# Kernel optimization log

Hardware: AMD Instinct MI355X
Metric: run time of the kernel (lower is better)

## Reference

```python
import jax, jax.numpy as jnp
import numpy as np
import math

B, L, D = 2, 2048, 512
H, HD = 8, 64                      # num_heads, head_dim = D // H
NG = D * (D - 1) // 2              # SO(D) generator count = 130816


def setup_inputs() -> dict:
    key = jax.random.key(0)
    ks = jax.random.split(key, 8)
    x = jax.random.normal(ks[0], (B, L, D), jnp.float32)
    # additive causal mask [L, L]
    mask = jnp.where(jnp.tril(jnp.ones((L, L), bool)), 0.0, -1e9).astype(jnp.float32)
    coef = lambda k: jax.random.normal(k, (NG,), jnp.float32) * 0.1
    basis = lambda k: jax.random.normal(k, (HD, HD), jnp.float32) * 0.1
    return {
        "x": x, "mask": mask,
        "coef_q": coef(ks[1]), "coef_k": coef(ks[2]),
        "coef_v": coef(ks[3]), "coef_o": coef(ks[4]),
        "bias_q": jnp.zeros((D,), jnp.float32), "bias_k": jnp.zeros((D,), jnp.float32),
        "bias_v": jnp.zeros((D,), jnp.float32), "bias_o": jnp.zeros((D,), jnp.float32),
        "basis_q": basis(ks[5]), "basis_k": basis(ks[6]),
    }


def _make_W(coefs):
    # W = I + sum_i coef_i * G_i, with G_i the antisymmetric basis (row-major i<j).
    iu = jnp.triu_indices(D, k=1)
    A = jnp.zeros((D, D), coefs.dtype).at[iu].set(coefs)
    return A - A.T + jnp.eye(D, dtype=coefs.dtype)


def _proj(x, coefs, bias):
    # F.linear(x, W, b) = x @ W.T + b
    return x @ _make_W(coefs).T + bias


def _invariants(t, basis):
    # t: [B, H, L, HD] -> concat(norm, t @ basis.T)[..., :HD]
    norm = jnp.linalg.norm(t, axis=-1, keepdims=True)
    ip = jnp.einsum('bhld,nd->bhln', t, basis)
    return jnp.concatenate([norm, ip], axis=-1)[..., :HD]


def reference(x, mask, coef_q, coef_k, coef_v, coef_o,
              bias_q, bias_k, bias_v, bias_o, basis_q, basis_k):
    split = lambda t: t.reshape(B, L, H, HD).transpose(0, 2, 1, 3)  # [B,H,L,HD]
    Q = split(_proj(x, coef_q, bias_q))
    K = split(_proj(x, coef_k, bias_k))
    V = split(_proj(x, coef_v, bias_v))
    Qi = _invariants(Q, basis_q)
    Ki = _invariants(K, basis_k)
    scores = jnp.einsum('bhld,bhmd->bhlm', Qi, Ki) / math.sqrt(HD) + mask
    attn = jax.nn.softmax(scores, axis=-1)
    out = jnp.einsum('bhlm,bhmd->bhld', attn, V)
    out = out.transpose(0, 2, 1, 3).reshape(B, L, D)
    return _proj(out, coef_o, bias_o)
```

## Files before the change

### kernel.cpp

```cpp
#include <hip/hip_runtime.h>
#include <hip/hip_bf16.h>
#include <math.h>

#define D_ 512
#define B_ 2
#define L_ 2048
#define H_ 8
#define HD_ 64

typedef __attribute__((ext_vector_type(8))) short short8;
typedef __attribute__((ext_vector_type(4))) float f32x4;

__device__ __forceinline__ ushort f2bf(float f) {
  __hip_bfloat16 h = __float2bfloat16(f);
  return *(ushort*)&h;
}
__device__ __forceinline__ float bf2f(ushort u) {
  unsigned int v = ((unsigned int)u) << 16;
  union { unsigned int u; float f; } c; c.u = v; return c.f;
}
__device__ __forceinline__ int swz(int row, int col) {
  return row*64 + (((col>>3) ^ (row&7))<<3) + (col&7);
}
__device__ __forceinline__ int tri_idx(int i, int j) {
  return i*(D_-1) - (i*(i-1))/2 + (j - i - 1);
}

#define GLL16(g, l) __builtin_amdgcn_global_load_lds( \
    (const __attribute__((address_space(1))) void*)(g), \
    (__attribute__((address_space(3))) void*)(l), 16, 0, 0)
#define GLL4(g, l) __builtin_amdgcn_global_load_lds( \
    (const __attribute__((address_space(1))) void*)(g), \
    (__attribute__((address_space(3))) void*)(l), 4, 0, 0)

__global__ void prep_kernel(const float* __restrict__ x,
                            const float* __restrict__ cq, const float* __restrict__ ck,
                            const float* __restrict__ cv, const float* __restrict__ co,
                            const float* __restrict__ basq, const float* __restrict__ bask,
                            ushort* __restrict__ xb, ushort* __restrict__ Wb,
                            ushort* __restrict__ Bq, ushort* __restrict__ Bk) {
  int blk = blockIdx.x, tid = threadIdx.x;
  if (blk < 2048) {
    int i = (blk*256 + tid)*4;
    float4 v = *(const float4*)(x + i);
    ushort4 o = make_ushort4(f2bf(v.x), f2bf(v.y), f2bf(v.z), f2bf(v.w));
    *(ushort4*)(xb + i) = o;
  } else if (blk < 6144) {
    int e = (blk-2048)*256 + tid;
    int m = e >> 18, n = (e>>9)&511, k = e&511;
    const float* cf = (m==0)?cq:(m==1)?ck:(m==2)?cv:co;
    float v = (k>n) ? cf[tri_idx(n,k)] : (k<n) ? -cf[tri_idx(k,n)] : 0.f;
    Wb[e] = f2bf(v);
  } else {
    int e = (blk-6144)*256 + tid;
    int which = e >> 12, ee = e & 4095;
    int n = ee >> 6, d = ee & 63;
    const float* bs = which ? bask : basq;
    float v = (n==0) ? 0.f : bs[(n-1)*64 + d];
    (which ? Bk : Bq)[ee] = f2bf(v);
  }
}

__global__ __launch_bounds__(256) void proj_kernel(
    const ushort* __restrict__ Xb, const float* __restrict__ Xf,
    const ushort* __restrict__ Wb,
    const float* __restrict__ bq, const float* __restrict__ bk,
    const float* __restrict__ bv, const float* __restrict__ bo,
    const ushort* __restrict__ Basq, const ushort* __restrict__ Bask,
    ushort* __restrict__ Qi_bf, float* __restrict__ Nq,
    ushort* __restrict__ Ki_bf, float* __restrict__ Nk,
    ushort* __restrict__ Vt_g, float* __restrict__ OutF,
    int mode_override)
{
  __shared__ ushort BufA[4096];
  __shared__ ushort BufB[4096];

  const int tid = threadIdx.x;
  const int lane = tid & 63, w = tid >> 6;
  const int lr = lane & 15, lg = lane >> 4;
  const int by = blockIdx.y;
  const int mode = (mode_override >= 0) ? mode_override : (by >> 6);
  const int mb   = (mode_override >= 0) ? by : (by & 63);
  const int h = blockIdx.x;
  const int n0 = h*64, m0 = mb*64;
  const ushort* Wm = Wb + (size_t)mode*262144;
  const float* bias = (mode==0)?bq:(mode==1)?bk:(mode==2)?bv:bo;

  f32x4 acc[4] = {};
  for (int k0 = 0; k0 < 512; k0 += 64) {
    __syncthreads();
    #pragma unroll
    for (int i = 0; i < 2; ++i) {
      int idx = tid + 256*i;
      int row = idx >> 3, c = idx & 7;
      *(short8*)&BufA[swz(row, c*8)] = *(const short8*)(Xb + (size_t)(m0+row)*512 + k0 + c*8);
      *(short8*)&BufB[swz(row, c*8)] = *(const short8*)(Wm + (size_t)(n0+row)*512 + k0 + c*8);
    }
    __syncthreads();
    short8 af[2];
    #pragma unroll
    for (int ks = 0; ks < 2; ++ks)
      af[ks] = *(const short8*)&BufA[swz(w*16+lr, (ks*4+lg)*8)];
    #pragma unroll
    for (int nb = 0; nb < 4; ++nb) {
      f32x4 a = acc[nb];
      #pragma unroll
      for (int ks = 0; ks < 2; ++ks) {
        short8 bfr = *(const short8*)&BufB[swz(nb*16+lr, (ks*4+lg)*8)];
        a = __builtin_amdgcn_mfma_f32_16x16x32_bf16(af[ks], bfr, a, 0,0,0);
      }
      acc[nb] = a;
    }
  }

  float bias4[4];
  #pragma unroll
  for (int nb = 0; nb < 4; ++nb) bias4[nb] = bias[n0 + nb*16 + lr];
  float q[4][4];
  #pragma unroll
  for (int nb = 0; nb < 4; ++nb)
    #pragma unroll
    for (int r = 0; r < 4; ++r) {
      size_t m = m0 + w*16 + lg*4 + r;
      size_t idx = m*512 + n0 + nb*16 + lr;
      float ex = Xf ? Xf[idx] : bf2f(Xb[idx]);
      q[nb][r] = ex + acc[nb][r] + bias4[nb];
    }

  if (mode == 2) {
    #pragma unroll
    for (int nb = 0; nb < 4; ++nb) {
      ushort4 o = make_ushort4(f2bf(q[nb][0]), f2bf(q[nb][1]), f2bf(q[nb][2]), f2bf(q[nb][3]));
      int b = m0 >> 11, l0 = (m0 & 2047) + w*16 + lg*4;
      size_t idx = (size_t)(b*8 + h)*131072 + (size_t)(nb*16 + lr)*2048 + l0;
      *(ushort4*)(Vt_g + idx) = o;
    }
    return;
  }
  if (mode == 3) {
    #pragma unroll
    for (int nb = 0; nb < 4; ++nb)
      #pragma unroll
      for (int r = 0; r < 4; ++r) {
        size_t m = m0 + w*16 + lg*4 + r;
        OutF[m*512 + n0 + nb*16 + lr] = q[nb][r];
      }
    return;
  }

  const float scale = (mode == 0) ? 0.125f : 1.0f;
  float norm[4];
  #pragma unroll
  for (int r = 0; r < 4; ++r) {
    float s = 0.f;
    #pragma unroll
    for (int nb = 0; nb < 4; ++nb) s = fmaf(q[nb][r], q[nb][r], s);
    s += __shfl_xor(s, 1, 16);
    s += __shfl_xor(s, 2, 16);
    s += __shfl_xor(s, 4, 16);
    s += __shfl_xor(s, 8, 16);
    norm[r] = sqrtf(s);
  }
  __syncthreads();
  {
    const ushort* Bsrc = (mode==0) ? Basq : Bask;
    #pragma unroll
    for (int i = 0; i < 2; ++i) {
      int idx = tid + 256*i;
      int row = idx >> 3, c = idx & 7;
      *(short8*)&BufB[swz(row, c*8)] = *(const short8*)(Bsrc + row*64 + c*8);
    }
  }
  #pragma unroll
  for (int nb = 0; nb < 4; ++nb)
    #pragma unroll
    for (int r = 0; r < 4; ++r)
      BufA[swz(w*16 + lg*4 + r, nb*16 + lr)] = f2bf(q[nb][r]);
  __syncthreads();

  f32x4 acc2[4] = {};
  short8 af2[2];
  #pragma unroll
  for (int ks = 0; ks < 2; ++ks)
    af2[ks] = *(const short8*)&BufA[swz(w*16+lr, (ks*4+lg)*8)];
  #pragma unroll
  for (int nb = 0; nb < 4; ++nb) {
    f32x4 a = acc2[nb];
    #pragma unroll
    for (int ks = 0; ks < 2; ++ks) {
      short8 bfr = *(const short8*)&BufB[swz(nb*16+lr, (ks*4+lg)*8)];
      a = __builtin_amdgcn_mfma_f32_16x16x32_bf16(af2[ks], bfr, a, 0,0,0);
    }
    acc2[nb] = a;
  }

  ushort* Qdst = (mode==0) ? Qi_bf : Ki_bf;
  float*  Ndst = (mode==0) ? Nq : Nk;
  int b = m0 >> 11;
  #pragma unroll
  for (int nb = 0; nb < 4; ++nb)
    #pragma unroll
    for (int r = 0; r < 4; ++r) {
      int ninv = nb*16 + lr;
      int l = (m0 & 2047) + w*16 + lg*4 + r;
      float v = acc2[nb][r] * scale;
      if (ninv == 0) v = 0.f;
      Qdst[((size_t)(b*8 + h)*2048 + l)*64 + ninv] = f2bf(v);
      if (lr == 0 && nb == 0) Ndst[(size_t)(b*8 + h)*2048 + l] = norm[r] * scale;
    }
}

__device__ __forceinline__ void stage_kv(const ushort* __restrict__ Kg,
                                         const ushort* __restrict__ Vg,
                                         const float* __restrict__ Nkg,
                                         ushort* Ksb, ushort* Vsb, float* Nkb,
                                         int w, int lane) {
  const int r8 = lane >> 3;
  const int cx = (lane & 7) ^ r8;
  #pragma unroll
  for (int s = 0; s < 2; ++s) {
    const int seg = w*2 + s;
    const int row = seg*8 + r8;
    GLL16(Kg + (size_t)row*64 + cx*8,   (char*)Ksb + seg*1024);
    GLL16(Vg + (size_t)row*2048 + cx*8, (char*)Vsb + seg*1024);
  }
  if (w == 0) GLL4(Nkg + lane, Nkb);
}

__global__ __launch_bounds__(256) void attn_kernel(
    const ushort* __restrict__ Qi_bf, const float* __restrict__ Nq,
    const ushort* __restrict__ Ki_bf, const float* __restrict__ Nk,
    const ushort* __restrict__ Vt_g, ushort* __restrict__ AO_bf)
{
  __shared__ ushort Ks[2][4096], Vt[2][4096], Pl[4096];
  __shared__ float NkS[2][64];

  const int tid = threadIdx.x;
  const int lane = tid & 63, w = tid >> 6;
  const int lr = lane & 15, lg = lane >> 4;
  const int blk = blockIdx.x;
  const int g  = blk >> 4;
  const int bh = blk & 15;
  const int qb = (g < 16) ? (31 - g) : (g - 16);
  const int b = bh >> 3, h = bh & 7;
  const ushort* Kg0 = Ki_bf + (size_t)bh*2048*64;
  const ushort* Vg0 = Vt_g + (size_t)bh*131072;
  const float*  Nkg = Nk + (size_t)bh*2048;
  const int prow = w*16 + lr;
  const int qg0 = qb*64;

  const ushort* qrow = Qi_bf + ((size_t)bh*2048 + qg0 + w*16 + lr)*64;
  short8 qf[2];
  qf[0] = *(const short8*)(qrow + lg*8);
  qf[1] = *(const short8*)(qrow + 32 + lg*8);
  const float nq = Nq[(size_t)bh*2048 + qg0 + w*16 + lr];

  float m_i = -1e30f, l_i = 0.f;
  f32x4 accO[4] = {};

  stage_kv(Kg0, Vg0, Nkg, Ks[0], Vt[0], NkS[0], w, lane);
  __syncthreads();

  for (int jb = 0; jb <= qb; ++jb) {
    const int cur = jb & 1;
    if (jb < qb)
      stage_kv(Kg0 + (size_t)(jb+1)*4096, Vg0 + (jb+1)*64, Nkg + (jb+1)*64,
               Ks[cur^1], Vt[cur^1], NkS[cur^1], w, lane);

    f32x4 sf[4];
    __builtin_amdgcn_s_setprio(1);
    #pragma unroll
    for (int cb = 0; cb < 4; ++cb) {
      f32x4 a = {0.f,0.f,0.f,0.f};
      #pragma unroll
      for (int ks = 0; ks < 2; ++ks) {
        short8 kfr = *(const short8*)&Ks[cur][swz(cb*16+lr, (ks*4+lg)*8)];
        a = __builtin_amdgcn_mfma_f32_16x16x32_bf16(kfr, qf[ks], a, 0,0,0);
      }
      sf[cb] = a;
    }
    __builtin_amdgcn_s_setprio(0);
    #pragma unroll
    for (int cb = 0; cb < 4; ++cb)
      #pragma unroll
      for (int r = 0; r < 4; ++r)
        sf[cb][r] += nq * NkS[cur][cb*16 + lg*4 + r];
    if (jb == qb) {
      #pragma unroll
      for (int cb = 0; cb < 4; ++cb)
        #pragma unroll
        for (int r = 0; r < 4; ++r)
          if (cb*16 + lg*4 + r > w*16 + lr) sf[cb][r] = -1e30f;
    }

    float mt = sf[0][0];
    #pragma unroll
    for (int cb = 0; cb < 4; ++cb)
      #pragma unroll
      for (int r = 0; r < 4; ++r) mt = fmaxf(mt, sf[cb][r]);
    mt = fmaxf(mt, __shfl_xor(mt, 16));
    mt = fmaxf(mt, __shfl_xor(mt, 32));
    float mn = fmaxf(m_i, mt);
    float sc = __expf(m_i - mn);
    m_i = mn;
    float p[4][4], rs = 0.f;
    #pragma unroll
    for (int cb = 0; cb < 4; ++cb)
      #pragma unroll
      for (int r = 0; r < 4; ++r) { p[cb][r] = __expf(sf[cb][r] - mn); rs += p[cb][r]; }
    rs += __shfl_xor(rs, 16);
    rs += __shfl_xor(rs, 32);
    l_i = l_i*sc + rs;
    #pragma unroll
    for (int db = 0; db < 4; ++db)
      #pragma unroll
      for (int r = 0; r < 4; ++r) accO[db][r] *= sc;

    #pragma unroll
    for (int cb = 0; cb < 4; ++cb) {
      ushort4 pk = make_ushort4(f2bf(p[cb][0]), f2bf(p[cb][1]), f2bf(p[cb][2]), f2bf(p[cb][3]));
      *(ushort4*)&Pl[swz(prow, cb*16 + lg*4)] = pk;
    }

    short8 pfr[2];
    #pragma unroll
    for (int ks = 0; ks < 2; ++ks)
      pfr[ks] = *(const short8*)&Pl[swz(prow, (ks*4+lg)*8)];
    __builtin_amdgcn_s_setprio(1);
    #pragma unroll
    for (int db = 0; db < 4; ++db) {
      f32x4 a = accO[db];
      #pragma unroll
      for (int ks = 0; ks < 2; ++ks) {
        short8 vfr = *(const short8*)&Vt[cur][swz(db*16+lr, (ks*4+lg)*8)];
        a = __builtin_amdgcn_mfma_f32_16x16x32_bf16(vfr, pfr[ks], a, 0,0,0);
      }
      accO[db] = a;
    }
    __builtin_amdgcn_s_setprio(0);
    __syncthreads();
  }

  const float inv = 1.0f / l_i;
  const int q = qg0 + w*16 + lr;
  #pragma unroll
  for (int db = 0; db < 4; ++db) {
    ushort4 o = make_ushort4(f2bf(accO[db][0]*inv), f2bf(accO[db][1]*inv),
                             f2bf(accO[db][2]*inv), f2bf(accO[db][3]*inv));
    *(ushort4*)(AO_bf + ((size_t)(b*2048 + q))*512 + h*64 + db*16 + lg*4) = o;
  }
}

extern "C" void kernel_launch(void* const* d_in, const int* in_sizes, int n_in,
                              void* d_out, int out_size, void* d_ws, size_t ws_size,
                              hipStream_t stream) {
  const float* x       = (const float*)d_in[0];
  const float* coef_q  = (const float*)d_in[2];
  const float* coef_k  = (const float*)d_in[3];
  const float* coef_v  = (const float*)d_in[4];
  const float* coef_o  = (const float*)d_in[5];
  const float* bias_q  = (const float*)d_in[6];
  const float* bias_k  = (const float*)d_in[7];
  const float* bias_v  = (const float*)d_in[8];
  const float* bias_o  = (const float*)d_in[9];
  const float* basis_q = (const float*)d_in[10];
  const float* basis_k = (const float*)d_in[11];
  float* out = (float*)d_out;

  ushort* xb    = (ushort*)d_ws;
  ushort* Wb    = xb + 2097152;
  ushort* Basq  = Wb + 1048576;
  ushort* Bask  = Basq + 4096;
  ushort* Qi_bf = Bask + 4096;
  ushort* Ki_bf = Qi_bf + 2097152;
  ushort* Vt_g  = Ki_bf + 2097152;
  ushort* AO_bf = Vt_g + 2097152;
  float*  Nq    = (float*)(AO_bf + 2097152);
  float*  Nk    = Nq + 32768;

  prep_kernel<<<dim3(6176), 256, 0, stream>>>(x, coef_q, coef_k, coef_v, coef_o,
                                              basis_q, basis_k, xb, Wb, Basq, Bask);

  proj_kernel<<<dim3(8, 192), 256, 0, stream>>>(xb, x, Wb,
      bias_q, bias_k, bias_v, bias_o, Basq, Bask,
      Qi_bf, Nq, Ki_bf, Nk, Vt_g, nullptr, -1);

  attn_kernel<<<dim3(512), 256, 0, stream>>>(Qi_bf, Nq, Ki_bf, Nk, Vt_g, AO_bf);

  proj_kernel<<<dim3(8, 64), 256, 0, stream>>>(AO_bf, nullptr, Wb,
      bias_q, bias_k, bias_v, bias_o, Basq, Bask,
      Qi_bf, Nq, Ki_bf, Nk, Vt_g, out, 3);
}
```

Baseline: 82.58 us.

## Load K/V fragments directly to registers and software-pipeline QK with softmax

Drops the LDS double-buffered K/V staging and the block-wide barriers. Each wave now loads its MFMA K and V fragments straight from global memory into registers, with the key norms loaded the same way. The loop is software-pipelined: the next tile's QK MFMAs are issued between the previous tile's softmax and its PV product, so matrix work overlaps the exp and reduction work. Each wave keeps a private P buffer in LDS, which removes inter-wave sync, but every wave now re-reads the same K/V tiles from global/L2 instead of sharing one staged copy, and register pressure goes up.

```diff
diff --git a/kernel.cpp b/kernel.cpp
--- a/kernel.cpp
+++ b/kernel.cpp
@@ -25,13 +25,6 @@
 __device__ __forceinline__ int tri_idx(int i, int j) {
   return i*(D_-1) - (i*(i-1))/2 + (j - i - 1);
 }
-
-#define GLL16(g, l) __builtin_amdgcn_global_load_lds( \
-    (const __attribute__((address_space(1))) void*)(g), \
-    (__attribute__((address_space(3))) void*)(l), 16, 0, 0)
-#define GLL4(g, l) __builtin_amdgcn_global_load_lds( \
-    (const __attribute__((address_space(1))) void*)(g), \
-    (__attribute__((address_space(3))) void*)(l), 4, 0, 0)
 
 __global__ void prep_kernel(const float* __restrict__ x,
                             const float* __restrict__ cq, const float* __restrict__ ck,
@@ -210,21 +203,100 @@
     }
 }
 
-__device__ __forceinline__ void stage_kv(const ushort* __restrict__ Kg,
-                                         const ushort* __restrict__ Vg,
-                                         const float* __restrict__ Nkg,
-                                         ushort* Ksb, ushort* Vsb, float* Nkb,
-                                         int w, int lane) {
-  const int r8 = lane >> 3;
-  const int cx = (lane & 7) ^ r8;
-  #pragma unroll
-  for (int s = 0; s < 2; ++s) {
-    const int seg = w*2 + s;
-    const int row = seg*8 + r8;
-    GLL16(Kg + (size_t)row*64 + cx*8,   (char*)Ksb + seg*1024);
-    GLL16(Vg + (size_t)row*2048 + cx*8, (char*)Vsb + seg*1024);
-  }
-  if (w == 0) GLL4(Nkg + lane, Nkb);
+__device__ __forceinline__ void load_k(const ushort* __restrict__ Kt,
+                                       int lr, int lg, short8 (&kf)[4][2]) {
+  #pragma unroll
+  for (int cb = 0; cb < 4; ++cb)
+    #pragma unroll
+    for (int ks = 0; ks < 2; ++ks)
+      kf[cb][ks] = *(const short8*)(Kt + (size_t)(cb*16 + lr)*64 + ks*32 + lg*8);
+}
+__device__ __forceinline__ void load_v(const ushort* __restrict__ Vt,
+                                       int lr, int lg, short8 (&vf)[4][2]) {
+  #pragma unroll
+  for (int db = 0; db < 4; ++db)
+    #pragma unroll
+    for (int ks = 0; ks < 2; ++ks)
+      vf[db][ks] = *(const short8*)(Vt + (size_t)(db*16 + lr)*2048 + ks*32 + lg*8);
+}
+__device__ __forceinline__ void qk_step(const short8 (&kf)[4][2],
+                                        const short8 &qf0, const short8 &qf1,
+                                        const f32x4 (&nkv)[4], const float nq,
+                                        f32x4 (&sf)[4]) {
+  __builtin_amdgcn_s_setprio(1);
+  #pragma unroll
+  for (int cb = 0; cb < 4; ++cb) {
+    f32x4 a = {0.f,0.f,0.f,0.f};
+    a = __builtin_amdgcn_mfma_f32_16x16x32_bf16(kf[cb][0], qf0, a, 0,0,0);
+    a = __builtin_amdgcn_mfma_f32_16x16x32_bf16(kf[cb][1], qf1, a, 0,0,0);
+    sf[cb] = a;
+  }
+  __builtin_amdgcn_s_setprio(0);
+  #pragma unroll
+  for (int cb = 0; cb < 4; ++cb)
+    #pragma unroll
+    for (int r = 0; r < 4; ++r)
+      sf[cb][r] += nq * nkv[cb][r];
+}
+__device__ __forceinline__ void softmax_step(f32x4 (&sf)[4], float &m_i, float &l_i,
+                                             f32x4 (&accO)[4], ushort* __restrict__ Plw,
+                                             int lr, int lg, int qloc, bool mask) {
+  if (mask) {
+    #pragma unroll
+    for (int cb = 0; cb < 4; ++cb)
+      #pragma unroll
+      for (int r = 0; r < 4; ++r)
+        if (cb*16 + lg*4 + r > qloc) sf[cb][r] = -1e30f;
+  }
+  float mt = sf[0][0];
+  #pragma unroll
+  for (int cb = 0; cb < 4; ++cb)
+    #pragma unroll
+    for (int r = 0; r < 4; ++r) mt = fmaxf(mt, sf[cb][r]);
+  mt = fmaxf(mt, __shfl_xor(mt, 16));
+  mt = fmaxf(mt, __shfl_xor(mt, 32));
+  float mn = fmaxf(m_i, mt);
+  float sc = __expf(m_i - mn);
+  m_i = mn;
+  float rs = 0.f;
+  #pragma unroll
+  for (int cb = 0; cb < 4; ++cb)
+    #pragma unroll
+    for (int r = 0; r < 4; ++r) {
+      float p = __expf(sf[cb][r] - mn);
+      rs += p;
+      sf[cb][r] = p;
+    }
+  rs += __shfl_xor(rs, 16);
+  rs += __shfl_xor(rs, 32);
+  l_i = l_i*sc + rs;
+  #pragma unroll
+  for (int db = 0; db < 4; ++db)
+    #pragma unroll
+    for (int r = 0; r < 4; ++r) accO[db][r] *= sc;
+  #pragma unroll
+  for (int cb = 0; cb < 4; ++cb) {
+    ushort4 pk = make_ushort4(f2bf(sf[cb][0]), f2bf(sf[cb][1]),
+                              f2bf(sf[cb][2]), f2bf(sf[cb][3]));
+    *(ushort4*)&Plw[swz(lr, cb*16 + lg*4)] = pk;
+  }
+}
+__device__ __forceinline__ void pv_step(const short8 (&vf)[4][2],
+                                        const ushort* __restrict__ Plw,
+                                        int lr, int lg, f32x4 (&accO)[4]) {
+  short8 pfr[2];
+  #pragma unroll
+  for (int ks = 0; ks < 2; ++ks)
+    pfr[ks] = *(const short8*)&Plw[swz(lr, (ks*4+lg)*8)];
+  __builtin_amdgcn_s_setprio(1);
+  #pragma unroll
+  for (int db = 0; db < 4; ++db) {
+    f32x4 a = accO[db];
+    a = __builtin_amdgcn_mfma_f32_16x16x32_bf16(vf[db][0], pfr[0], a, 0,0,0);
+    a = __builtin_amdgcn_mfma_f32_16x16x32_bf16(vf[db][1], pfr[1], a, 0,0,0);
+    accO[db] = a;
+  }
+  __builtin_amdgcn_s_setprio(0);
 }
 
 __global__ __launch_bounds__(256) void attn_kernel(
@@ -232,8 +304,7 @@
     const ushort* __restrict__ Ki_bf, const float* __restrict__ Nk,
     const ushort* __restrict__ Vt_g, ushort* __restrict__ AO_bf)
 {
-  __shared__ ushort Ks[2][4096], Vt[2][4096], Pl[4096];
-  __shared__ float NkS[2][64];
+  __shared__ ushort Pl[4][1024];
 
   const int tid = threadIdx.x;
   const int lane = tid & 63, w = tid >> 6;
@@ -243,106 +314,48 @@
   const int bh = blk & 15;
   const int qb = (g < 16) ? (31 - g) : (g - 16);
   const int b = bh >> 3, h = bh & 7;
-  const ushort* Kg0 = Ki_bf + (size_t)bh*2048*64;
+  const ushort* Kg0 = Ki_bf + (size_t)bh*131072;
   const ushort* Vg0 = Vt_g + (size_t)bh*131072;
   const float*  Nkg = Nk + (size_t)bh*2048;
-  const int prow = w*16 + lr;
   const int qg0 = qb*64;
-
-  const ushort* qrow = Qi_bf + ((size_t)bh*2048 + qg0 + w*16 + lr)*64;
-  short8 qf[2];
-  qf[0] = *(const short8*)(qrow + lg*8);
-  qf[1] = *(const short8*)(qrow + 32 + lg*8);
-  const float nq = Nq[(size_t)bh*2048 + qg0 + w*16 + lr];
+  const int qloc = w*16 + lr;
+  ushort* Plw = Pl[w];
+
+  const ushort* qrow = Qi_bf + ((size_t)bh*2048 + qg0 + qloc)*64;
+  const short8 qf0 = *(const short8*)(qrow + lg*8);
+  const short8 qf1 = *(const short8*)(qrow + 32 + lg*8);
+  const float nq = Nq[(size_t)bh*2048 + qg0 + qloc];
 
   float m_i = -1e30f, l_i = 0.f;
   f32x4 accO[4] = {};
-
-  stage_kv(Kg0, Vg0, Nkg, Ks[0], Vt[0], NkS[0], w, lane);
-  __syncthreads();
-
-  for (int jb = 0; jb <= qb; ++jb) {
-    const int cur = jb & 1;
-    if (jb < qb)
-      stage_kv(Kg0 + (size_t)(jb+1)*4096, Vg0 + (jb+1)*64, Nkg + (jb+1)*64,
-               Ks[cur^1], Vt[cur^1], NkS[cur^1], w, lane);
-
-    f32x4 sf[4];
-    __builtin_amdgcn_s_setprio(1);
-    #pragma unroll
-    for (int cb = 0; cb < 4; ++cb) {
-      f32x4 a = {0.f,0.f,0.f,0.f};
-      #pragma unroll
-      for (int ks = 0; ks < 2; ++ks) {
-        short8 kfr = *(const short8*)&Ks[cur][swz(cb*16+lr, (ks*4+lg)*8)];
-        a = __builtin_amdgcn_mfma_f32_16x16x32_bf16(kfr, qf[ks], a, 0,0,0);
-      }
-      sf[cb] = a;
-    }
-    __builtin_amdgcn_s_setprio(0);
+  short8 kf[4][2], vf[4][2];
+  f32x4 sf_prev[4], sf_cur[4], nkv[4];
+
+  load_k(Kg0, lr, lg, kf);
+  #pragma unroll
+  for (int cb = 0; cb < 4; ++cb)
+    nkv[cb] = *(const f32x4*)(Nkg + cb*16 + lg*4);
+  qk_step(kf, qf0, qf1, nkv, nq, sf_prev);
+  load_v(Vg0, lr, lg, vf);
+
+  for (int jb = 1; jb <= qb; ++jb) {
+    load_k(Kg0 + (size_t)jb*4096, lr, lg, kf);
     #pragma unroll
     for (int cb = 0; cb < 4; ++cb)
-      #pragma unroll
-      for (int r = 0; r < 4; ++r)
-        sf[cb][r] += nq * NkS[cur][cb*16 + lg*4 + r];
-    if (jb == qb) {
-      #pragma unroll
-      for (int cb = 0; cb < 4; ++cb)
-        #pragma unroll
-        for (int r = 0; r < 4; ++r)
-          if (cb*16 + lg*4 + r > w*16 + lr) sf[cb][r] = -1e30f;
-    }
-
-    float mt = sf[0][0];
-    #pragma unroll
-    for (int cb = 0; cb < 4; ++cb)
-      #pragma unroll
-      for (int r = 0; r < 4; ++r) mt = fmaxf(mt, sf[cb][r]);
-    mt = fmaxf(mt, __shfl_xor(mt, 16));
-    mt = fmaxf(mt, __shfl_xor(mt, 32));
-    float mn = fmaxf(m_i, mt);
-    float sc = __expf(m_i - mn);
-    m_i = mn;
-    float p[4][4], rs = 0.f;
-    #pragma unroll
-    for (int cb = 0; cb < 4; ++cb)
-      #pragma unroll
-      for (int r = 0; r < 4; ++r) { p[cb][r] = __expf(sf[cb][r] - mn); rs += p[cb][r]; }
-    rs += __shfl_xor(rs, 16);
-    rs += __shfl_xor(rs, 32);
-    l_i = l_i*sc + rs;
-    #pragma unroll
-    for (int db = 0; db < 4; ++db)
-      #pragma unroll
-      for (int r = 0; r < 4; ++r) accO[db][r] *= sc;
-
-    #pragma unroll
-    for (int cb = 0; cb < 4; ++cb) {
-      ushort4 pk = make_ushort4(f2bf(p[cb][0]), f2bf(p[cb][1]), f2bf(p[cb][2]), f2bf(p[cb][3]));
-      *(ushort4*)&Pl[swz(prow, cb*16 + lg*4)] = pk;
-    }
-
-    short8 pfr[2];
-    #pragma unroll
-    for (int ks = 0; ks < 2; ++ks)
-      pfr[ks] = *(const short8*)&Pl[swz(prow, (ks*4+lg)*8)];
-    __builtin_amdgcn_s_setprio(1);
-    #pragma unroll
-    for (int db = 0; db < 4; ++db) {
-      f32x4 a = accO[db];
-      #pragma unroll
-      for (int ks = 0; ks < 2; ++ks) {
-        short8 vfr = *(const short8*)&Vt[cur][swz(db*16+lr, (ks*4+lg)*8)];
-        a = __builtin_amdgcn_mfma_f32_16x16x32_bf16(vfr, pfr[ks], a, 0,0,0);
-      }
-      accO[db] = a;
-    }
-    __builtin_amdgcn_s_setprio(0);
-    __syncthreads();
-  }
+      nkv[cb] = *(const f32x4*)(Nkg + jb*64 + cb*16 + lg*4);
+    softmax_step(sf_prev, m_i, l_i, accO, Plw, lr, lg, qloc, false);
+    qk_step(kf, qf0, qf1, nkv, nq, sf_cur);
+    pv_step(vf, Plw, lr, lg, accO);
+    load_v(Vg0 + (size_t)jb*64, lr, lg, vf);
+    #pragma unroll
+    for (int cb = 0; cb < 4; ++cb) sf_prev[cb] = sf_cur[cb];
+  }
+
+  softmax_step(sf_prev, m_i, l_i, accO, Plw, lr, lg, qloc, true);
+  pv_step(vf, Plw, lr, lg, accO);
 
   const float inv = 1.0f / l_i;
-  const int q = qg0 + w*16 + lr;
+  const int q = qg0 + qloc;
   #pragma unroll
   for (int db = 0; db < 4; ++db) {
     ushort4 o = make_ushort4(f2bf(accO[db][0]*inv), f2bf(accO[db][1]*inv),
```

Result: slower. 103.5 us (+25.3%).

## Use split-bf16 hi/lo products for invariants and scores with static softmax bound

Applied to the files above, without the earlier changes.

The invariant projection and the QK score matmul now use a split-bf16 (hi+lo) scheme with three MFMA products, which roughly triples those matmuls and doubles Q/K storage and loads. This is meant to raise accuracy. The online softmax rescaling is replaced by a fixed per-row upper bound built from Cauchy-Schwarz norm maxima, which removes the per-tile max reductions and accumulator rescales. The attention output is now stored in fp32 and converted to bf16 during the output projection's load. The main intent looks like accuracy, with the softmax simplification offsetting part of the extra cost.

```diff
diff --git a/kernel.cpp b/kernel.cpp
--- a/kernel.cpp
+++ b/kernel.cpp
@@ -38,7 +38,8 @@
                             const float* __restrict__ cv, const float* __restrict__ co,
                             const float* __restrict__ basq, const float* __restrict__ bask,
                             ushort* __restrict__ xb, ushort* __restrict__ Wb,
-                            ushort* __restrict__ Bq, ushort* __restrict__ Bk) {
+                            ushort* __restrict__ Bqh, ushort* __restrict__ Bql,
+                            ushort* __restrict__ Bkh, ushort* __restrict__ Bkl) {
   int blk = blockIdx.x, tid = threadIdx.x;
   if (blk < 2048) {
     int i = (blk*256 + tid)*4;
@@ -57,7 +58,10 @@
     int n = ee >> 6, d = ee & 63;
     const float* bs = which ? bask : basq;
     float v = (n==0) ? 0.f : bs[(n-1)*64 + d];
-    (which ? Bk : Bq)[ee] = f2bf(v);
+    ushort hi = f2bf(v);
+    ushort lo = f2bf(v - bf2f(hi));
+    if (which) { Bkh[ee] = hi; Bkl[ee] = lo; }
+    else       { Bqh[ee] = hi; Bql[ee] = lo; }
   }
 }
 
@@ -66,14 +70,19 @@
     const ushort* __restrict__ Wb,
     const float* __restrict__ bq, const float* __restrict__ bk,
     const float* __restrict__ bv, const float* __restrict__ bo,
-    const ushort* __restrict__ Basq, const ushort* __restrict__ Bask,
-    ushort* __restrict__ Qi_bf, float* __restrict__ Nq,
-    ushort* __restrict__ Ki_bf, float* __restrict__ Nk,
+    const ushort* __restrict__ Bqh, const ushort* __restrict__ Bql,
+    const ushort* __restrict__ Bkh, const ushort* __restrict__ Bkl,
+    ushort* __restrict__ QhO, ushort* __restrict__ QlO,
+    float* __restrict__ Nq, float* __restrict__ Nqr,
+    ushort* __restrict__ KhO, ushort* __restrict__ KlO,
+    float* __restrict__ Nk, float* __restrict__ Nkr,
     ushort* __restrict__ Vt_g, float* __restrict__ OutF,
     int mode_override)
 {
   __shared__ ushort BufA[4096];
   __shared__ ushort BufB[4096];
+  __shared__ ushort BufC[4096];
+  __shared__ ushort BufD[4096];
 
   const int tid = threadIdx.x;
   const int lane = tid & 63, w = tid >> 6;
@@ -93,7 +102,15 @@
     for (int i = 0; i < 2; ++i) {
       int idx = tid + 256*i;
       int row = idx >> 3, c = idx & 7;
-      *(short8*)&BufA[swz(row, c*8)] = *(const short8*)(Xb + (size_t)(m0+row)*512 + k0 + c*8);
+      if (Xb) {
+        *(short8*)&BufA[swz(row, c*8)] = *(const short8*)(Xb + (size_t)(m0+row)*512 + k0 + c*8);
+      } else {
+        const float* s = Xf + (size_t)(m0+row)*512 + k0 + c*8;
+        float4 a = *(const float4*)s, b2 = *(const float4*)(s+4);
+        ushort u[8] = {f2bf(a.x),f2bf(a.y),f2bf(a.z),f2bf(a.w),
+                       f2bf(b2.x),f2bf(b2.y),f2bf(b2.z),f2bf(b2.w)};
+        *(short8*)&BufA[swz(row, c*8)] = *(short8*)u;
+      }
       *(short8*)&BufB[swz(row, c*8)] = *(const short8*)(Wm + (size_t)(n0+row)*512 + k0 + c*8);
     }
     __syncthreads();
@@ -163,40 +180,59 @@
   }
   __syncthreads();
   {
-    const ushort* Bsrc = (mode==0) ? Basq : Bask;
+    const ushort* Bh = (mode==0) ? Bqh : Bkh;
+    const ushort* Bl = (mode==0) ? Bql : Bkl;
     #pragma unroll
     for (int i = 0; i < 2; ++i) {
       int idx = tid + 256*i;
       int row = idx >> 3, c = idx & 7;
-      *(short8*)&BufB[swz(row, c*8)] = *(const short8*)(Bsrc + row*64 + c*8);
+      *(short8*)&BufB[swz(row, c*8)] = *(const short8*)(Bh + row*64 + c*8);
+      *(short8*)&BufD[swz(row, c*8)] = *(const short8*)(Bl + row*64 + c*8);
     }
   }
   #pragma unroll
   for (int nb = 0; nb < 4; ++nb)
     #pragma unroll
-    for (int r = 0; r < 4; ++r)
-      BufA[swz(w*16 + lg*4 + r, nb*16 + lr)] = f2bf(q[nb][r]);
+    for (int r = 0; r < 4; ++r) {
+      float v = q[nb][r];
+      ushort hi = f2bf(v);
+      ushort lo = f2bf(v - bf2f(hi));
+      BufA[swz(w*16 + lg*4 + r, nb*16 + lr)] = hi;
+      BufC[swz(w*16 + lg*4 + r, nb*16 + lr)] = lo;
+    }
   __syncthreads();
 
   f32x4 acc2[4] = {};
-  short8 af2[2];
-  #pragma unroll
-  for (int ks = 0; ks < 2; ++ks)
-    af2[ks] = *(const short8*)&BufA[swz(w*16+lr, (ks*4+lg)*8)];
+  short8 ah[2], al[2];
+  #pragma unroll
+  for (int ks = 0; ks < 2; ++ks) {
+    ah[ks] = *(const short8*)&BufA[swz(w*16+lr, (ks*4+lg)*8)];
+    al[ks] = *(const short8*)&BufC[swz(w*16+lr, (ks*4+lg)*8)];
+  }
   #pragma unroll
   for (int nb = 0; nb < 4; ++nb) {
     f32x4 a = acc2[nb];
-    #pragma unroll
-    for (int ks = 0; ks < 2; ++ks) {
-      short8 bfr = *(const short8*)&BufB[swz(nb*16+lr, (ks*4+lg)*8)];
-      a = __builtin_amdgcn_mfma_f32_16x16x32_bf16(af2[ks], bfr, a, 0,0,0);
-    }
+    short8 bh0 = *(const short8*)&BufB[swz(nb*16+lr, (0*4+lg)*8)];
+    short8 bh1 = *(const short8*)&BufB[swz(nb*16+lr, (1*4+lg)*8)];
+    short8 bl0 = *(const short8*)&BufD[swz(nb*16+lr, (0*4+lg)*8)];
+    short8 bl1 = *(const short8*)&BufD[swz(nb*16+lr, (1*4+lg)*8)];
+    a = __builtin_amdgcn_mfma_f32_16x16x32_bf16(ah[0], bh0, a, 0,0,0);
+    a = __builtin_amdgcn_mfma_f32_16x16x32_bf16(ah[1], bh1, a, 0,0,0);
+    a = __builtin_amdgcn_mfma_f32_16x16x32_bf16(al[0], bh0, a, 0,0,0);
+    a = __builtin_amdgcn_mfma_f32_16x16x32_bf16(al[1], bh1, a, 0,0,0);
+    a = __builtin_amdgcn_mfma_f32_16x16x32_bf16(ah[0], bl0, a, 0,0,0);
+    a = __builtin_amdgcn_mfma_f32_16x16x32_bf16(ah[1], bl1, a, 0,0,0);
     acc2[nb] = a;
   }
 
-  ushort* Qdst = (mode==0) ? Qi_bf : Ki_bf;
-  float*  Ndst = (mode==0) ? Nq : Nk;
+  ushort* dstH = (mode==0) ? QhO : KhO;
+  ushort* dstL = (mode==0) ? QlO : KlO;
+  float*  NdA  = (mode==0) ? Nq  : Nk;
+  float*  NdR  = (mode==0) ? Nqr : Nkr;
   int b = m0 >> 11;
+  float rn[4];
+  #pragma unroll
+  for (int r = 0; r < 4; ++r) rn[r] = 0.f;
   #pragma unroll
   for (int nb = 0; nb < 4; ++nb)
     #pragma unroll
@@ -205,34 +241,54 @@
       int l = (m0 & 2047) + w*16 + lg*4 + r;
       float v = acc2[nb][r] * scale;
       if (ninv == 0) v = 0.f;
-      Qdst[((size_t)(b*8 + h)*2048 + l)*64 + ninv] = f2bf(v);
-      if (lr == 0 && nb == 0) Ndst[(size_t)(b*8 + h)*2048 + l] = norm[r] * scale;
-    }
-}
-
-__device__ __forceinline__ void stage_kv(const ushort* __restrict__ Kg,
+      rn[r] = fmaf(v, v, rn[r]);
+      ushort hi = f2bf(v);
+      ushort lo = f2bf(v - bf2f(hi));
+      dstH[((size_t)(b*8 + h)*2048 + l)*64 + ninv] = hi;
+      dstL[((size_t)(b*8 + h)*2048 + l)*64 + ninv] = lo;
+    }
+  #pragma unroll
+  for (int r = 0; r < 4; ++r) {
+    float s = rn[r];
+    s += __shfl_xor(s, 1, 16);
+    s += __shfl_xor(s, 2, 16);
+    s += __shfl_xor(s, 4, 16);
+    s += __shfl_xor(s, 8, 16);
+    if (lr == 0) {
+      int l = (m0 & 2047) + w*16 + lg*4 + r;
+      NdA[(size_t)(b*8 + h)*2048 + l] = norm[r] * scale;
+      NdR[(size_t)(b*8 + h)*2048 + l] = sqrtf(s);
+    }
+  }
+}
+
+__device__ __forceinline__ void stage_kv(const ushort* __restrict__ Khg,
+                                         const ushort* __restrict__ Klg,
                                          const ushort* __restrict__ Vg,
                                          const float* __restrict__ Nkg,
-                                         ushort* Ksb, ushort* Vsb, float* Nkb,
-                                         int w, int lane) {
+                                         ushort* KhB, ushort* KlB, ushort* VB,
+                                         float* NkB, int w, int lane) {
   const int r8 = lane >> 3;
   const int cx = (lane & 7) ^ r8;
   #pragma unroll
   for (int s = 0; s < 2; ++s) {
     const int seg = w*2 + s;
     const int row = seg*8 + r8;
-    GLL16(Kg + (size_t)row*64 + cx*8,   (char*)Ksb + seg*1024);
-    GLL16(Vg + (size_t)row*2048 + cx*8, (char*)Vsb + seg*1024);
-  }
-  if (w == 0) GLL4(Nkg + lane, Nkb);
+    GLL16(Khg + (size_t)row*64 + cx*8,   (char*)KhB + seg*1024);
+    GLL16(Klg + (size_t)row*64 + cx*8,   (char*)KlB + seg*1024);
+    GLL16(Vg  + (size_t)row*2048 + cx*8, (char*)VB + seg*1024);
+  }
+  if (w == 0) GLL4(Nkg + lane, NkB);
 }
 
 __global__ __launch_bounds__(256) void attn_kernel(
-    const ushort* __restrict__ Qi_bf, const float* __restrict__ Nq,
-    const ushort* __restrict__ Ki_bf, const float* __restrict__ Nk,
-    const ushort* __restrict__ Vt_g, ushort* __restrict__ AO_bf)
+    const ushort* __restrict__ Qh_g, const ushort* __restrict__ Ql_g,
+    const float* __restrict__ Nq, const float* __restrict__ Nqr,
+    const ushort* __restrict__ Kh_g, const ushort* __restrict__ Kl_g,
+    const float* __restrict__ Nk, const float* __restrict__ Nkr,
+    const ushort* __restrict__ Vt_g, float* __restrict__ AO)
 {
-  __shared__ ushort Ks[2][4096], Vt[2][4096], Pl[4096];
+  __shared__ ushort KhS[2][4096], KlS[2][4096], VtS[2][4096], Pl[4096];
   __shared__ float NkS[2][64];
 
   const int tid = threadIdx.x;
@@ -243,40 +299,64 @@
   const int bh = blk & 15;
   const int qb = (g < 16) ? (31 - g) : (g - 16);
   const int b = bh >> 3, h = bh & 7;
-  const ushort* Kg0 = Ki_bf + (size_t)bh*2048*64;
+  const ushort* Khg = Kh_g + (size_t)bh*131072;
+  const ushort* Klg = Kl_g + (size_t)bh*131072;
   const ushort* Vg0 = Vt_g + (size_t)bh*131072;
-  const float*  Nkg = Nk + (size_t)bh*2048;
+  const float*  Nkg = Nk  + (size_t)bh*2048;
+  const float*  Nkrg = Nkr + (size_t)bh*2048;
+  const int qg0 = qb*64;
+  const int qloc = w*16 + lr;
   const int prow = w*16 + lr;
-  const int qg0 = qb*64;
-
-  const ushort* qrow = Qi_bf + ((size_t)bh*2048 + qg0 + w*16 + lr)*64;
-  short8 qf[2];
-  qf[0] = *(const short8*)(qrow + lg*8);
-  qf[1] = *(const short8*)(qrow + 32 + lg*8);
-  const float nq = Nq[(size_t)bh*2048 + qg0 + w*16 + lr];
-
-  float m_i = -1e30f, l_i = 0.f;
+
+  const size_t qoff = ((size_t)bh*2048 + qg0 + qloc)*64;
+  const short8 qh0 = *(const short8*)(Qh_g + qoff + lg*8);
+  const short8 qh1 = *(const short8*)(Qh_g + qoff + 32 + lg*8);
+  const short8 ql0 = *(const short8*)(Ql_g + qoff + lg*8);
+  const short8 ql1 = *(const short8*)(Ql_g + qoff + 32 + lg*8);
+  const float nq  = Nq[(size_t)bh*2048 + qg0 + qloc];
+  const float nqr = Nqr[(size_t)bh*2048 + qg0 + qloc];
+
+  float mk = -1e30f, mkr = -1e30f;
+  const int nkeys = qg0 + 64;
+  for (int jj = lane; jj < nkeys; jj += 64) {
+    mk  = fmaxf(mk,  Nkg[jj]);
+    mkr = fmaxf(mkr, Nkrg[jj]);
+  }
+  #pragma unroll
+  for (int off = 1; off < 64; off <<= 1) {
+    mk  = fmaxf(mk,  __shfl_xor(mk,  off));
+    mkr = fmaxf(mkr, __shfl_xor(mkr, off));
+  }
+  const float m_ub = nq*mk + nqr*mkr;
+
+  float l_lane = 0.f;
   f32x4 accO[4] = {};
 
-  stage_kv(Kg0, Vg0, Nkg, Ks[0], Vt[0], NkS[0], w, lane);
+  stage_kv(Khg, Klg, Vg0, Nkg, KhS[0], KlS[0], VtS[0], NkS[0], w, lane);
   __syncthreads();
 
   for (int jb = 0; jb <= qb; ++jb) {
     const int cur = jb & 1;
     if (jb < qb)
-      stage_kv(Kg0 + (size_t)(jb+1)*4096, Vg0 + (jb+1)*64, Nkg + (jb+1)*64,
-               Ks[cur^1], Vt[cur^1], NkS[cur^1], w, lane);
+      stage_kv(Khg + (size_t)(jb+1)*4096, Klg + (size_t)(jb+1)*4096,
+               Vg0 + (jb+1)*64, Nkg + (jb+1)*64,
+               KhS[cur^1], KlS[cur^1], VtS[cur^1], NkS[cur^1], w, lane);
 
     f32x4 sf[4];
     __builtin_amdgcn_s_setprio(1);
     #pragma unroll
     for (int cb = 0; cb < 4; ++cb) {
       f32x4 a = {0.f,0.f,0.f,0.f};
-      #pragma unroll
-      for (int ks = 0; ks < 2; ++ks) {
-        short8 kfr = *(const short8*)&Ks[cur][swz(cb*16+lr, (ks*4+lg)*8)];
-        a = __builtin_amdgcn_mfma_f32_16x16x32_bf16(kfr, qf[ks], a, 0,0,0);
-      }
+      short8 kh0 = *(const short8*)&KhS[cur][swz(cb*16+lr, lg*8)];
+      short8 kh1 = *(const short8*)&KhS[cur][swz(cb*16+lr, (4+lg)*8)];
+      short8 kl0 = *(const short8*)&KlS[cur][swz(cb*16+lr, lg*8)];
+      short8 kl1 = *(const short8*)&KlS[cur][swz(cb*16+lr, (4+lg)*8)];
+      a = __builtin_amdgcn_mfma_f32_16x16x32_bf16(kh0, qh0, a, 0,0,0);
+      a = __builtin_amdgcn_mfma_f32_16x16x32_bf16(kh1, qh1, a, 0,0,0);
+      a = __builtin_amdgcn_mfma_f32_16x16x32_bf16(kl0, qh0, a, 0,0,0);
+      a = __builtin_amdgcn_mfma_f32_16x16x32_bf16(kl1, qh1, a, 0,0,0);
+      a = __builtin_amdgcn_mfma_f32_16x16x32_bf16(kh0, ql0, a, 0,0,0);
+      a = __builtin_amdgcn_mfma_f32_16x16x32_bf16(kh1, ql1, a, 0,0,0);
       sf[cb] = a;
     }
     __builtin_amdgcn_s_setprio(0);
@@ -290,35 +370,21 @@
       for (int cb = 0; cb < 4; ++cb)
         #pragma unroll
         for (int r = 0; r < 4; ++r)
-          if (cb*16 + lg*4 + r > w*16 + lr) sf[cb][r] = -1e30f;
-    }
-
-    float mt = sf[0][0];
+          if (cb*16 + lg*4 + r > qloc) sf[cb][r] = -1e30f;
+    }
+
     #pragma unroll
     for (int cb = 0; cb < 4; ++cb)
       #pragma unroll
-      for (int r = 0; r < 4; ++r) mt = fmaxf(mt, sf[cb][r]);
-    mt = fmaxf(mt, __shfl_xor(mt, 16));
-    mt = fmaxf(mt, __shfl_xor(mt, 32));
-    float mn = fmaxf(m_i, mt);
-    float sc = __expf(m_i - mn);
-    m_i = mn;
-    float p[4][4], rs = 0.f;
-    #pragma unroll
-    for (int cb = 0; cb < 4; ++cb)
-      #pragma unroll
-      for (int r = 0; r < 4; ++r) { p[cb][r] = __expf(sf[cb][r] - mn); rs += p[cb][r]; }
-    rs += __shfl_xor(rs, 16);
-    rs += __shfl_xor(rs, 32);
-    l_i = l_i*sc + rs;
-    #pragma unroll
-    for (int db = 0; db < 4; ++db)
-      #pragma unroll
-      for (int r = 0; r < 4; ++r) accO[db][r] *= sc;
-
+      for (int r = 0; r < 4; ++r) {
+        float p = __expf(sf[cb][r] - m_ub);
+        l_lane += p;
+        sf[cb][r] = p;
+      }
     #pragma unroll
     for (int cb = 0; cb < 4; ++cb) {
-      ushort4 pk = make_ushort4(f2bf(p[cb][0]), f2bf(p[cb][1]), f2bf(p[cb][2]), f2bf(p[cb][3]));
+      ushort4 pk = make_ushort4(f2bf(sf[cb][0]), f2bf(sf[cb][1]),
+                                f2bf(sf[cb][2]), f2bf(sf[cb][3]));
       *(ushort4*)&Pl[swz(prow, cb*16 + lg*4)] = pk;
     }
 
@@ -330,24 +396,26 @@
     #pragma unroll
     for (int db = 0; db < 4; ++db) {
       f32x4 a = accO[db];
-      #pragma unroll
-      for (int ks = 0; ks < 2; ++ks) {
-        short8 vfr = *(const short8*)&Vt[cur][swz(db*16+lr, (ks*4+lg)*8)];
-        a = __builtin_amdgcn_mfma_f32_16x16x32_bf16(vfr, pfr[ks], a, 0,0,0);
-      }
+      short8 v0 = *(const short8*)&VtS[cur][swz(db*16+lr, lg*8)];
+      short8 v1 = *(const short8*)&VtS[cur][swz(db*16+lr, (4+lg)*8)];
+      a = __builtin_amdgcn_mfma_f32_16x16x32_bf16(v0, pfr[0], a, 0,0,0);
+      a = __builtin_amdgcn_mfma_f32_16x16x32_bf16(v1, pfr[1], a, 0,0,0);
       accO[db] = a;
     }
     __builtin_amdgcn_s_setprio(0);
     __syncthreads();
   }
 
-  const float inv = 1.0f / l_i;
-  const int q = qg0 + w*16 + lr;
+  l_lane += __shfl_xor(l_lane, 16);
+  l_lane += __shfl_xor(l_lane, 32);
+  const float inv = 1.0f / l_lane;
+  const int q = qg0 + qloc;
   #pragma unroll
   for (int db = 0; db < 4; ++db) {
-    ushort4 o = make_ushort4(f2bf(accO[db][0]*inv), f2bf(accO[db][1]*inv),
-                             f2bf(accO[db][2]*inv), f2bf(accO[db][3]*inv));
-    *(ushort4*)(AO_bf + ((size_t)(b*2048 + q))*512 + h*64 + db*16 + lg*4) = o;
+    f32x4 o;
+    #pragma unroll
+    for (int r = 0; r < 4; ++r) o[r] = accO[db][r]*inv;
+    *(f32x4*)(AO + ((size_t)(b*2048 + q))*512 + h*64 + db*16 + lg*4) = o;
   }
 }
 
@@ -367,27 +435,35 @@
   const float* basis_k = (const float*)d_in[11];
   float* out = (float*)d_out;
 
-  ushort* xb    = (ushort*)d_ws;
-  ushort* Wb    = xb + 2097152;
-  ushort* Basq  = Wb + 1048576;
-  ushort* Bask  = Basq + 4096;
-  ushort* Qi_bf = Bask + 4096;
-  ushort* Ki_bf = Qi_bf + 2097152;
-  ushort* Vt_g  = Ki_bf + 2097152;
-  ushort* AO_bf = Vt_g + 2097152;
-  float*  Nq    = (float*)(AO_bf + 2097152);
-  float*  Nk    = Nq + 32768;
+  ushort* xb   = (ushort*)d_ws;
+  ushort* Wb   = xb + 2097152;
+  ushort* Bqh  = Wb + 1048576;
+  ushort* Bql  = Bqh + 4096;
+  ushort* Bkh  = Bql + 4096;
+  ushort* Bkl  = Bkh + 4096;
+  ushort* Qh   = Bkl + 4096;
+  ushort* Ql   = Qh + 2097152;
+  ushort* Kh   = Ql + 2097152;
+  ushort* Kl   = Kh + 2097152;
+  ushort* Vt_g = Kl + 2097152;
+  float*  AO   = (float*)(Vt_g + 2097152);
+  float*  Nq   = AO + 2097152;
+  float*  Nqr  = Nq + 32768;
+  float*  Nk   = Nqr + 32768;
+  float*  Nkr  = Nk + 32768;
 
   prep_kernel<<<dim3(6176), 256, 0, stream>>>(x, coef_q, coef_k, coef_v, coef_o,
-                                              basis_q, basis_k, xb, Wb, Basq, Bask);
+                                              basis_q, basis_k, xb, Wb,
+                                              Bqh, Bql, Bkh, Bkl);
 
   proj_kernel<<<dim3(8, 192), 256, 0, stream>>>(xb, x, Wb,
-      bias_q, bias_k, bias_v, bias_o, Basq, Bask,
-      Qi_bf, Nq, Ki_bf, Nk, Vt_g, nullptr, -1);
-
-  attn_kernel<<<dim3(512), 256, 0, stream>>>(Qi_bf, Nq, Ki_bf, Nk, Vt_g, AO_bf);
-
-  proj_kernel<<<dim3(8, 64), 256, 0, stream>>>(AO_bf, nullptr, Wb,
-      bias_q, bias_k, bias_v, bias_o, Basq, Bask,
-      Qi_bf, Nq, Ki_bf, Nk, Vt_g, out, 3);
-}
+      bias_q, bias_k, bias_v, bias_o, Bqh, Bql, Bkh, Bkl,
+      Qh, Ql, Nq, Nqr, Kh, Kl, Nk, Nkr, Vt_g, nullptr, -1);
+
+  attn_kernel<<<dim3(512), 256, 0, stream>>>(Qh, Ql, Nq, Nqr,
+                                             Kh, Kl, Nk, Nkr, Vt_g, AO);
+
+  proj_kernel<<<dim3(8, 64), 256, 0, stream>>>(nullptr, AO, Wb,
+      bias_q, bias_k, bias_v, bias_o, Bqh, Bql, Bkh, Bkl,
+      Qh, Ql, Nq, Nqr, Kh, Kl, Nk, Nkr, Vt_g, out, 3);
+}
```

After: 112.5 us. 36.2% more time.
